# Optimization experiments

Measured on AMD Instinct MI355X. Metric: run time of the kernel, lower is better.

The kernel has to match this reference:

```python
import jax, jax.numpy as jnp
import numpy as np

EPS = 1e-5
NUM_GRAPHS = 32

def _bn(x, g, b):
    # BatchNorm1d, training mode: biased batch stats over the node axis
    mu = x.mean(0)
    var = ((x - mu) ** 2).mean(0)
    return g * (x - mu) * jax.lax.rsqrt(var + EPS) + b

def setup_inputs() -> dict:
    key = jax.random.key(0)
    ks = jax.random.split(key, 12)
    G, S, deg, D, L = 32, 1024, 32, 128, 4
    N, E = G * S, G * S * deg
    # within-graph random edges (proxy for radius_graph, no self-loops)
    rng = np.random.default_rng(0)
    col = np.repeat(np.arange(N), deg)                      # targets (x_i)
    src_local = (col % S + 1 + rng.integers(0, S - 1, size=E)) % S
    row = (col // S) * S + src_local                        # sources (x_j)
    edge_index = jnp.asarray(np.stack([row, col]).astype(np.int32))
    z = jax.random.randint(ks[0], (N,), 0, 100, dtype=jnp.int32)
    pos = jax.random.uniform(ks[1], (N, 3), dtype=jnp.float32) * 10.0
    batch = jnp.repeat(jnp.arange(G, dtype=jnp.int32), S)
    s_in = 1.0 / np.sqrt(2 * D + 1)
    s_d = 1.0 / np.sqrt(D)
    return {
        "z": z, "pos": pos, "batch": batch, "edge_index": edge_index,
        "emb": jax.random.normal(ks[2], (100, D), jnp.float32),
        "Wf": jax.random.normal(ks[3], (L, 2 * D + 1, D), jnp.float32) * s_in,
        "bf": jnp.zeros((L, D), jnp.float32),
        "Ws": jax.random.normal(ks[4], (L, 2 * D + 1, D), jnp.float32) * s_in,
        "bs": jnp.zeros((L, D), jnp.float32),
        "gc": jnp.ones((L, D), jnp.float32),
        "bc": jnp.zeros((L, D), jnp.float32),
        "gn": jnp.ones((L, D), jnp.float32),
        "bn_b": jnp.zeros((L, D), jnp.float32),
        "W1": jax.random.normal(ks[5], (D, D), jnp.float32) * s_d,
        "b1": jnp.zeros((D,), jnp.float32),
        "W2": jax.random.normal(ks[6], (D, 1), jnp.float32) * s_d,
        "b2": jnp.zeros((1,), jnp.float32),
    }

def reference(z, pos, batch, edge_index, emb, Wf, bf, Ws, bs, gc, bc, gn, bn_b, W1, b1, W2, b2):
    x = emb[z]                                              # [N, D]
    row, col = edge_index[0], edge_index[1]                 # j (src), i (tgt)
    dist = jnp.linalg.norm(pos[row] - pos[col], axis=-1, keepdims=True)  # [E,1]
    N = x.shape[0]
    for l in range(Wf.shape[0]):
        # CGConv message: cat([x_i, x_j, edge_attr]) -> gated softplus
        ze = jnp.concatenate([x[col], x[row], dist], axis=-1)  # [E, 2D+1]
        msg = jax.nn.sigmoid(ze @ Wf[l] + bf[l]) * jax.nn.softplus(ze @ Ws[l] + bs[l])
        agg = jax.ops.segment_sum(msg, col, num_segments=N)    # scatter-add to targets
        x = _bn(agg, gc[l], bc[l]) + x                         # CGConv internal BN + residual
        x = jax.nn.relu(_bn(x, gn[l], bn_b[l]))                # outer BN + ReLU (dropout=0)
    cnt = jax.ops.segment_sum(jnp.ones((N, 1), x.dtype), batch, num_segments=NUM_GRAPHS)
    g = jax.ops.segment_sum(x, batch, num_segments=NUM_GRAPHS) / cnt  # global_mean_pool
    h = jax.nn.relu(g @ W1 + b1)
    return (h @ W2 + b2).reshape(-1)
```

## Files before the change

kernel.cpp:

```cpp
#include <hip/hip_runtime.h>
#include <math.h>

#define D 128
#define LOG2E 1.44269504f

typedef short bf16x8 __attribute__((ext_vector_type(8)));
typedef float f32x4 __attribute__((ext_vector_type(4)));
typedef float f4 __attribute__((ext_vector_type(4)));
typedef unsigned short u16x4 __attribute__((ext_vector_type(4)));

__device__ __forceinline__ unsigned short f2bf(float f) {
    unsigned int u = __float_as_uint(f);
    u += 0x7fff + ((u >> 16) & 1);
    return (unsigned short)(u >> 16);
}
__device__ __forceinline__ float bf2f(unsigned short h) {
    return __uint_as_float(((unsigned int)h) << 16);
}
__device__ __forceinline__ bf16x8 load_bf8(const unsigned short* p) {
    return __builtin_bit_cast(bf16x8, *reinterpret_cast<const uint4*>(p));
}
__device__ __forceinline__ float exp2_hw(float x) {
    float r; asm("v_exp_f32 %0, %1" : "=v"(r) : "v"(x)); return r;
}
__device__ __forceinline__ float log2_hw(float x) {
    float r; asm("v_log_f32 %0, %1" : "=v"(r) : "v"(x)); return r;
}

__device__ __forceinline__ int swz_node0(int gi, int S, int G) {
    if ((G & 7) == 0 && (S & 7) == 0) {
        int xcd = gi & 7, i = gi >> 3;
        int bpg = S >> 3;
        int gr = i / bpg, li = i - gr * bpg;
        return (xcd + 8 * gr) * S + li * 8;
    }
    return gi * 8;
}

__global__ __launch_bounds__(256) void k_embed(const int* __restrict__ z,
        const float* __restrict__ emb, float* __restrict__ x,
        unsigned short* __restrict__ xh, unsigned short* __restrict__ xl, int N) {
    int idx = blockIdx.x * blockDim.x + threadIdx.x;
    if (idx >= N * 32) return;
    int n = idx >> 5;
    int d0 = (idx & 31) * 4;
    f4 v = *reinterpret_cast<const f4*>(emb + (size_t)z[n] * D + d0);
    *reinterpret_cast<f4*>(x + (size_t)n * D + d0) = v;
    u16x4 h, l;
    #pragma unroll
    for (int c = 0; c < 4; c++) {
        h[c] = f2bf(v[c]);
        l[c] = f2bf(v[c] - bf2f(h[c]));
    }
    *reinterpret_cast<u16x4*>(xh + (size_t)n * D + d0) = h;
    *reinterpret_cast<u16x4*>(xl + (size_t)n * D + d0) = l;
}

__global__ void k_dist(const int* __restrict__ row, const int* __restrict__ col,
                       const float* __restrict__ pos, int2* __restrict__ jd, int E) {
    int e = blockIdx.x * blockDim.x + threadIdx.x;
    if (e >= E) return;
    int r = row[e], c = col[e];
    float dx = pos[3 * r + 0] - pos[3 * c + 0];
    float dy = pos[3 * r + 1] - pos[3 * c + 1];
    float dz = pos[3 * r + 2] - pos[3 * c + 2];
    float dist = sqrtf(dx * dx + dy * dy + dz * dz);
    jd[e] = make_int2(r, __float_as_int(dist));
}

__global__ void k_cvtW(const float* __restrict__ Wf, const float* __restrict__ Ws,
                       unsigned short* __restrict__ Wth, unsigned short* __restrict__ Wtl,
                       int L) {
    int idx = blockIdx.x * blockDim.x + threadIdx.x;
    if (idx >= L * 4 * D * D) return;
    int k = idx & 127;
    int n = (idx >> 7) & 127;
    int mat = (idx >> 14) & 3;
    int l = idx >> 16;
    const float* src = (mat < 2) ? Wf : Ws;
    float scale = (mat < 2) ? -LOG2E : LOG2E;
    float v = scale * src[(size_t)l * 257 * D + (size_t)((mat & 1) * D + k) * D + n];
    unsigned short h = f2bf(v);
    Wth[idx] = h;
    Wtl[idx] = f2bf(v - bf2f(h));
}

__global__ __launch_bounds__(256) void k_gemm_mfma(
        const unsigned short* __restrict__ Xh, const unsigned short* __restrict__ Xl,
        const unsigned short* __restrict__ Wth, const unsigned short* __restrict__ Wtl,
        const float* __restrict__ bfl, const float* __restrict__ bsl,
        float* __restrict__ AfAs, float* __restrict__ BfBs, int S, int G) {
    int pair = blockIdx.y;
    float* O0 = AfAs + (pair ? 128 : 0);
    float* O1 = BfBs + (pair ? 128 : 0);
    const float* bias = pair ? bsl : bfl;
    float bsc = pair ? LOG2E : -LOG2E;
    const unsigned short* W0 = Wth + (size_t)(2 * pair) * D * D;
    const unsigned short* W1 = Wth + (size_t)(2 * pair + 1) * D * D;

    int wave = threadIdx.x >> 6;
    int lane = threadIdx.x & 63;
    int r16 = lane & 15;
    int kg = lane >> 4;

    int xb = blockIdx.x;
    int tile0;
    if ((G & 7) == 0 && (S & 127) == 0) {
        int xcd = xb & 7, i = xb >> 3;
        int tpg = S >> 7;
        int gi = i / tpg, t = i - gi * tpg;
        tile0 = (xcd + 8 * gi) * S + t * 128;
    } else tile0 = xb * 128;
    int row0 = tile0 + (wave >> 1) * 64;
    int wc = (wave & 1) * 64;

    f32x4 acc0[4][4], acc1[4][4];
    #pragma unroll
    for (int m = 0; m < 4; m++)
        #pragma unroll
        for (int n = 0; n < 4; n++) {
            acc0[m][n] = (f32x4){0.f, 0.f, 0.f, 0.f};
            acc1[m][n] = (f32x4){0.f, 0.f, 0.f, 0.f};
        }

    #pragma unroll
    for (int ks = 0; ks < 4; ++ks) {
        int k0 = ks * 32 + kg * 8;
        bf16x8 ah[4], al[4], b0[4], b1[4];
        #pragma unroll
        for (int m = 0; m < 4; m++) {
            size_t off = (size_t)(row0 + m * 16 + r16) * D + k0;
            ah[m] = load_bf8(Xh + off);
            al[m] = load_bf8(Xl + off);
        }
        #pragma unroll
        for (int n = 0; n < 4; n++) {
            size_t off = (size_t)(wc + n * 16 + r16) * D + k0;
            b0[n] = load_bf8(W0 + off);
            b1[n] = load_bf8(W1 + off);
        }
        #pragma unroll
        for (int m = 0; m < 4; m++)
            #pragma unroll
            for (int n = 0; n < 4; n++) {
                acc0[m][n] = __builtin_amdgcn_mfma_f32_16x16x32_bf16(ah[m], b0[n], acc0[m][n], 0, 0, 0);
                acc0[m][n] = __builtin_amdgcn_mfma_f32_16x16x32_bf16(al[m], b0[n], acc0[m][n], 0, 0, 0);
                acc1[m][n] = __builtin_amdgcn_mfma_f32_16x16x32_bf16(ah[m], b1[n], acc1[m][n], 0, 0, 0);
                acc1[m][n] = __builtin_amdgcn_mfma_f32_16x16x32_bf16(al[m], b1[n], acc1[m][n], 0, 0, 0);
            }
    }

    #pragma unroll
    for (int n = 0; n < 4; n++) {
        int col = wc + n * 16 + r16;
        float bv = bias[col] * bsc;
        #pragma unroll
        for (int m = 0; m < 4; m++) {
            int rbase = row0 + m * 16 + kg * 4;
            #pragma unroll
            for (int r = 0; r < 4; r++) {
                O0[(size_t)(rbase + r) * 256 + col] = acc0[m][n][r] + bv;
                O1[(size_t)(rbase + r) * 256 + col] = acc1[m][n][r];
            }
        }
    }
}

__global__ __launch_bounds__(256) void k_edges(
        const int2* __restrict__ jd,
        const float* __restrict__ AfAs, const float* __restrict__ BfBs,
        const float* __restrict__ wfd, const float* __restrict__ wsd,
        const float* __restrict__ x,
        float* __restrict__ agg, float* __restrict__ st, int N, int S, int G, int deg) {
    __shared__ int2 jds[512];
    __shared__ f4 sred[256];
    __shared__ f4 sredq[256];
    int b = blockIdx.x;
    int node0 = swz_node0(b, S, G);
    int tid = threadIdx.x;
    int grp = tid >> 5, lane = tid & 31;
    bool use_lds = (8 * deg) <= 512;
    if (use_lds) {
        int tot = 8 * deg;
        int lim = (node0 + 8 <= N) ? tot : (N > node0 ? (N - node0) * deg : 0);
        for (int t = tid; t < lim; t += 256) jds[t] = jd[(size_t)node0 * deg + t];
    }
    __syncthreads();
    int node = node0 + grp;
    bool active = node < N;
    int d0 = lane * 4;
    f4 acc = {0.f, 0.f, 0.f, 0.f};
    f4 xv = {0.f, 0.f, 0.f, 0.f};
    if (active) {
        const f4 af4 = *reinterpret_cast<const f4*>(AfAs + (size_t)node * 256 + d0);
        const f4 as4 = *reinterpret_cast<const f4*>(AfAs + (size_t)node * 256 + 128 + d0);
        const f4 wf4 = *reinterpret_cast<const f4*>(wfd + d0) * (-LOG2E);
        const f4 ws4 = *reinterpret_cast<const f4*>(wsd + d0) * (LOG2E);
        const int2* jrow = use_lds ? (jds + grp * deg) : (jd + (size_t)node * deg);
        #pragma unroll 8
        for (int e = 0; e < deg; e++) {
            int2 p = jrow[e];
            float dst = __int_as_float(p.y);
            int off = (p.x << 8) + d0;
            f4 bf4 = *reinterpret_cast<const f4*>(BfBs + off);
            f4 bs4 = *reinterpret_cast<const f4*>(BfBs + off + 128);
            #pragma unroll
            for (int c = 0; c < 4; c++) {
                float u2 = fmaf(dst, wf4[c], af4[c]) + bf4[c];
                float v2 = fmaf(dst, ws4[c], as4[c]) + bs4[c];
                float sE = exp2_hw(u2);
                float tE = exp2_hw(v2);
                float sg = __builtin_amdgcn_rcpf(1.0f + sE);
                float sp = log2_hw(1.0f + tE);
                acc[c] = fmaf(sg, sp, acc[c]);
            }
        }
        *reinterpret_cast<f4*>(agg + (size_t)node * D + d0) = acc;
        xv = *reinterpret_cast<const f4*>(x + (size_t)node * D + d0);
    }
    float* stb = st + (b & 7) * 640;
    sred[tid] = acc;
    sredq[tid] = acc * acc;
    __syncthreads();
    if (tid < 64) {
        int which = tid >> 5, l = tid & 31;
        f4 s = which ? sredq[l] : sred[l];
        #pragma unroll
        for (int g = 1; g < 8; g++) s += which ? sredq[g * 32 + l] : sred[g * 32 + l];
        float* dstp = stb + which * 128;
        #pragma unroll
        for (int c = 0; c < 4; c++) atomicAdd(dstp + l * 4 + c, s[c]);
    }
    __syncthreads();
    sred[tid] = xv;
    sredq[tid] = xv * xv;
    __syncthreads();
    if (tid < 64) {
        int which = tid >> 5, l = tid & 31;
        f4 s = which ? sredq[l] : sred[l];
        #pragma unroll
        for (int g = 1; g < 8; g++) s += which ? sredq[g * 32 + l] : sred[g * 32 + l];
        float* dstp = stb + 256 + which * 128;
        #pragma unroll
        for (int c = 0; c < 4; c++) atomicAdd(dstp + l * 4 + c, s[c]);
    }
    __syncthreads();
    sred[tid] = acc * xv;
    __syncthreads();
    if (tid < 32) {
        f4 s = sred[tid];
        #pragma unroll
        for (int g = 1; g < 8; g++) s += sred[g * 32 + tid];
        #pragma unroll
        for (int c = 0; c < 4; c++) atomicAdd(stb + 512 + tid * 4 + c, s[c]);
    }
}

__global__ __launch_bounds__(256) void k_bnfused(
        const float* __restrict__ st,
        const float* __restrict__ gc, const float* __restrict__ bc,
        const float* __restrict__ gn, const float* __restrict__ bnb,
        const float* __restrict__ agg, float* __restrict__ x,
        unsigned short* __restrict__ xh, unsigned short* __restrict__ xl,
        int N, int S, int G) {
    int tid = threadIdx.x;
    int lane = tid & 31, grp = tid >> 5;
    int d0 = lane * 4;
    int node = swz_node0(blockIdx.x, S, G) + grp;
    if (node >= N) return;
    float invN = 1.0f / (float)N;
    f4 Sa = {0.f, 0.f, 0.f, 0.f}, Sa2 = {0.f, 0.f, 0.f, 0.f};
    f4 Sx = {0.f, 0.f, 0.f, 0.f}, Sx2 = {0.f, 0.f, 0.f, 0.f}, Sax = {0.f, 0.f, 0.f, 0.f};
    #pragma unroll
    for (int r = 0; r < 8; r++) {
        const float* stb = st + r * 640;
        Sa  += *reinterpret_cast<const f4*>(stb + d0);
        Sa2 += *reinterpret_cast<const f4*>(stb + 128 + d0);
        Sx  += *reinterpret_cast<const f4*>(stb + 256 + d0);
        Sx2 += *reinterpret_cast<const f4*>(stb + 384 + d0);
        Sax += *reinterpret_cast<const f4*>(stb + 512 + d0);
    }
    f4 g1 = *reinterpret_cast<const f4*>(gc + d0);
    f4 b1v = *reinterpret_cast<const f4*>(bc + d0);
    f4 g2 = *reinterpret_cast<const f4*>(gn + d0);
    f4 b2v = *reinterpret_cast<const f4*>(bnb + d0);
    f4 A, C, mu2, inv2;
    #pragma unroll
    for (int c = 0; c < 4; c++) {
        float m1 = Sa[c] * invN;
        float var1 = Sa2[c] * invN - m1 * m1;
        float i1 = rsqrtf(var1 + 1e-5f);
        float a = g1[c] * i1;
        float cc = b1v[c] - a * m1;
        float mx = Sx[c] * invN;
        float m2 = b1v[c] + mx;
        float e2 = (a * a * Sa2[c] + 2.f * a * cc * Sa[c] + 2.f * a * Sax[c]
                    + 2.f * cc * Sx[c] + Sx2[c]) * invN + cc * cc;
        float var2 = e2 - m2 * m2;
        A[c] = a; C[c] = cc; mu2[c] = m2;
        inv2[c] = rsqrtf(var2 + 1e-5f);
    }
    size_t idx = (size_t)node * D + d0;
    f4 av = *reinterpret_cast<const f4*>(agg + idx);
    f4 xv = *reinterpret_cast<const f4*>(x + idx);
    f4 o;
    u16x4 h, l;
    #pragma unroll
    for (int c = 0; c < 4; c++) {
        float xn = fmaf(A[c], av[c], C[c]) + xv[c];
        float t = fmaf(g2[c] * (xn - mu2[c]), inv2[c], b2v[c]);
        t = fmaxf(t, 0.0f);
        o[c] = t;
        h[c] = f2bf(t);
        l[c] = f2bf(t - bf2f(h[c]));
    }
    *reinterpret_cast<f4*>(x + idx) = o;
    *reinterpret_cast<u16x4*>(xh + idx) = h;
    *reinterpret_cast<u16x4*>(xl + idx) = l;
}

__global__ __launch_bounds__(256) void k_pool(const float* __restrict__ x,
        float* __restrict__ gsum, int S, int G) {
    __shared__ f4 s[256];
    int b = blockIdx.x;
    int g, sub;
    if ((G & 31) == 0) { g = b & 31; sub = b >> 5; }
    else               { g = b >> 3; sub = b & 7; }
    int tid = threadIdx.x;
    int grp = tid >> 5, lane = tid & 31;
    int d0 = lane * 4;
    f4 a = {0.f, 0.f, 0.f, 0.f};
    for (int r = sub * 8 + grp; r < S; r += 64)
        a += *reinterpret_cast<const f4*>(x + ((size_t)g * S + r) * D + d0);
    s[tid] = a;
    __syncthreads();
    if (tid < 32) {
        f4 acc = s[tid];
        #pragma unroll
        for (int q = 1; q < 8; q++) acc += s[q * 32 + tid];
        #pragma unroll
        for (int c = 0; c < 4; c++) atomicAdd(&gsum[g * D + tid * 4 + c], acc[c]);
    }
}

__global__ __launch_bounds__(128) void k_mlp(const float* __restrict__ gsum,
        const float* __restrict__ W1, const float* __restrict__ b1,
        const float* __restrict__ W2, const float* __restrict__ b2,
        float* __restrict__ out, int S) {
    __shared__ float gm[D];
    __shared__ float red[128];
    int g = blockIdx.x, d = threadIdx.x;
    gm[d] = gsum[g * D + d] / (float)S;
    __syncthreads();
    float h = b1[d];
    #pragma unroll 8
    for (int k = 0; k < D; k++) h = fmaf(gm[k], W1[k * D + d], h);
    h = fmaxf(h, 0.0f);
    red[d] = h * W2[d];
    __syncthreads();
    for (int st = 64; st > 0; st >>= 1) {
        if (d < st) red[d] += red[d + st];
        __syncthreads();
    }
    if (d == 0) out[g] = red[0] + b2[0];
}

extern "C" void kernel_launch(void* const* d_in, const int* in_sizes, int n_in,
                              void* d_out, int out_size, void* d_ws, size_t ws_size,
                              hipStream_t stream) {
    const int*   z    = (const int*)d_in[0];
    const float* pos  = (const float*)d_in[1];
    const int*   eidx = (const int*)d_in[3];
    const float* emb  = (const float*)d_in[4];
    const float* Wf   = (const float*)d_in[5];
    const float* bf   = (const float*)d_in[6];
    const float* Ws   = (const float*)d_in[7];
    const float* bs   = (const float*)d_in[8];
    const float* gc   = (const float*)d_in[9];
    const float* bc   = (const float*)d_in[10];
    const float* gn   = (const float*)d_in[11];
    const float* bnb  = (const float*)d_in[12];
    const float* W1   = (const float*)d_in[13];
    const float* b1   = (const float*)d_in[14];
    const float* W2   = (const float*)d_in[15];
    const float* b2   = (const float*)d_in[16];

    int N = in_sizes[0];
    int E = in_sizes[3] / 2;
    int L = in_sizes[6] / D;
    int deg = E / N;
    int G = out_size;
    int S = N / G;

    const int* row = eidx;
    const int* col = eidx + E;

    float* ws = (float*)d_ws;
    size_t nd = (size_t)N * D;
    float* x    = ws;
    float* AfAs = x + nd;
    float* BfBs = AfAs + 2 * nd;
    float* agg  = BfBs + 2 * nd;
    int2*  jd   = (int2*)(agg + nd);
    unsigned short* xh  = (unsigned short*)(jd + E);
    unsigned short* xl  = xh + nd;
    unsigned short* Wth = xl + nd;
    unsigned short* Wtl = Wth + (size_t)L * 4 * D * D;
    float* stats = (float*)(Wtl + (size_t)L * 4 * D * D);
    float* gsum  = stats + (size_t)L * 5120;

    hipMemsetAsync(stats, 0, ((size_t)L * 5120 + (size_t)G * D) * sizeof(float), stream);

    k_cvtW<<<(L * 4 * D * D + 255) / 256, 256, 0, stream>>>(Wf, Ws, Wth, Wtl, L);
    k_embed<<<(N * 32 + 255) / 256, 256, 0, stream>>>(z, emb, x, xh, xl, N);
    k_dist<<<(E + 255) / 256, 256, 0, stream>>>(row, col, pos, jd, E);

    int NG = (N + 7) / 8;
    for (int l = 0; l < L; ++l) {
        const float* Wfl = Wf + (size_t)l * 257 * D;
        const float* Wsl = Ws + (size_t)l * 257 * D;
        float* stp = stats + (size_t)l * 5120;
        k_gemm_mfma<<<dim3(N / 128, 2), 256, 0, stream>>>(
            xh, xl, Wth + (size_t)l * 4 * D * D, Wtl + (size_t)l * 4 * D * D,
            bf + l * D, bs + l * D, AfAs, BfBs, S, G);
        k_edges<<<NG, 256, 0, stream>>>(jd, AfAs, BfBs, Wfl + 256 * D, Wsl + 256 * D,
                                        x, agg, stp, N, S, G, deg);
        k_bnfused<<<NG, 256, 0, stream>>>(stp, gc + l * D, bc + l * D,
                                          gn + l * D, bnb + l * D,
                                          agg, x, xh, xl, N, S, G);
    }
    k_pool<<<G * 8, 256, 0, stream>>>(x, gsum, S, G);
    k_mlp<<<G, 128, 0, stream>>>(gsum, W1, b1, W2, b2, (float*)d_out, S);
}
```

Measured before the change: 550.4 us.

## Merge setup kernels into one launch and pack edge math into float2 ops

Folds the embedding, edge-distance and weight-conversion kernels into a single k_setup launch that dispatches on block index, removing two kernel launches and their gaps. The edge index is stored pre-multiplied by 256, so the edge loop drops a shift. The per-edge pre-activation math is rewritten as two-wide float vectors so the compiler can emit packed FP32 FMA/add instructions. Any gain is limited to launch overhead and a few VALU ops inside an edge loop that is likely bound by the transcendental functions or memory.

Result: no change. 547.1 us (-0.6%).

```diff
diff --git a/kernel.cpp b/kernel.cpp
--- a/kernel.cpp
+++ b/kernel.cpp
@@ -7,6 +7,7 @@
 typedef short bf16x8 __attribute__((ext_vector_type(8)));
 typedef float f32x4 __attribute__((ext_vector_type(4)));
 typedef float f4 __attribute__((ext_vector_type(4)));
+typedef float f2v __attribute__((ext_vector_type(2)));
 typedef unsigned short u16x4 __attribute__((ext_vector_type(4)));
 
 __device__ __forceinline__ unsigned short f2bf(float f) {
@@ -37,52 +38,54 @@
     return gi * 8;
 }
 
-__global__ __launch_bounds__(256) void k_embed(const int* __restrict__ z,
-        const float* __restrict__ emb, float* __restrict__ x,
-        unsigned short* __restrict__ xh, unsigned short* __restrict__ xl, int N) {
-    int idx = blockIdx.x * blockDim.x + threadIdx.x;
-    if (idx >= N * 32) return;
-    int n = idx >> 5;
-    int d0 = (idx & 31) * 4;
-    f4 v = *reinterpret_cast<const f4*>(emb + (size_t)z[n] * D + d0);
-    *reinterpret_cast<f4*>(x + (size_t)n * D + d0) = v;
-    u16x4 h, l;
-    #pragma unroll
-    for (int c = 0; c < 4; c++) {
-        h[c] = f2bf(v[c]);
-        l[c] = f2bf(v[c] - bf2f(h[c]));
-    }
-    *reinterpret_cast<u16x4*>(xh + (size_t)n * D + d0) = h;
-    *reinterpret_cast<u16x4*>(xl + (size_t)n * D + d0) = l;
-}
-
-__global__ void k_dist(const int* __restrict__ row, const int* __restrict__ col,
-                       const float* __restrict__ pos, int2* __restrict__ jd, int E) {
-    int e = blockIdx.x * blockDim.x + threadIdx.x;
-    if (e >= E) return;
-    int r = row[e], c = col[e];
-    float dx = pos[3 * r + 0] - pos[3 * c + 0];
-    float dy = pos[3 * r + 1] - pos[3 * c + 1];
-    float dz = pos[3 * r + 2] - pos[3 * c + 2];
-    float dist = sqrtf(dx * dx + dy * dy + dz * dz);
-    jd[e] = make_int2(r, __float_as_int(dist));
-}
-
-__global__ void k_cvtW(const float* __restrict__ Wf, const float* __restrict__ Ws,
-                       unsigned short* __restrict__ Wth, unsigned short* __restrict__ Wtl,
-                       int L) {
-    int idx = blockIdx.x * blockDim.x + threadIdx.x;
-    if (idx >= L * 4 * D * D) return;
-    int k = idx & 127;
-    int n = (idx >> 7) & 127;
-    int mat = (idx >> 14) & 3;
-    int l = idx >> 16;
-    const float* src = (mat < 2) ? Wf : Ws;
-    float scale = (mat < 2) ? -LOG2E : LOG2E;
-    float v = scale * src[(size_t)l * 257 * D + (size_t)((mat & 1) * D + k) * D + n];
-    unsigned short h = f2bf(v);
-    Wth[idx] = h;
-    Wtl[idx] = f2bf(v - bf2f(h));
+__global__ __launch_bounds__(256) void k_setup(
+        const int* __restrict__ z, const float* __restrict__ emb,
+        float* __restrict__ x, unsigned short* __restrict__ xh,
+        unsigned short* __restrict__ xl,
+        const int* __restrict__ row, const int* __restrict__ col,
+        const float* __restrict__ pos, int2* __restrict__ jd,
+        const float* __restrict__ Wf, const float* __restrict__ Ws,
+        unsigned short* __restrict__ Wth, unsigned short* __restrict__ Wtl,
+        int N, int E, int L, int nb_embed, int nb_dist) {
+    int b = blockIdx.x;
+    if (b < nb_embed) {
+        int idx = b * 256 + threadIdx.x;
+        if (idx >= N * 32) return;
+        int n = idx >> 5;
+        int d0 = (idx & 31) * 4;
+        f4 v = *reinterpret_cast<const f4*>(emb + (size_t)z[n] * D + d0);
+        *reinterpret_cast<f4*>(x + (size_t)n * D + d0) = v;
+        u16x4 h, l;
+        #pragma unroll
+        for (int c = 0; c < 4; c++) {
+            h[c] = f2bf(v[c]);
+            l[c] = f2bf(v[c] - bf2f(h[c]));
+        }
+        *reinterpret_cast<u16x4*>(xh + (size_t)n * D + d0) = h;
+        *reinterpret_cast<u16x4*>(xl + (size_t)n * D + d0) = l;
+    } else if (b < nb_embed + nb_dist) {
+        int e = (b - nb_embed) * 256 + threadIdx.x;
+        if (e >= E) return;
+        int r = row[e], c = col[e];
+        float dx = pos[3 * r + 0] - pos[3 * c + 0];
+        float dy = pos[3 * r + 1] - pos[3 * c + 1];
+        float dz = pos[3 * r + 2] - pos[3 * c + 2];
+        float dist = sqrtf(dx * dx + dy * dy + dz * dz);
+        jd[e] = make_int2(r * 256, __float_as_int(dist));
+    } else {
+        int idx = (b - nb_embed - nb_dist) * 256 + threadIdx.x;
+        if (idx >= L * 4 * D * D) return;
+        int k = idx & 127;
+        int n = (idx >> 7) & 127;
+        int mat = (idx >> 14) & 3;
+        int l = idx >> 16;
+        const float* src = (mat < 2) ? Wf : Ws;
+        float scale = (mat < 2) ? -LOG2E : LOG2E;
+        float v = scale * src[(size_t)l * 257 * D + (size_t)((mat & 1) * D + k) * D + n];
+        unsigned short h = f2bf(v);
+        Wth[idx] = h;
+        Wtl[idx] = f2bf(v - bf2f(h));
+    }
 }
 
 __global__ __launch_bounds__(256) void k_gemm_mfma(
@@ -196,20 +199,33 @@
         const f4 as4 = *reinterpret_cast<const f4*>(AfAs + (size_t)node * 256 + 128 + d0);
         const f4 wf4 = *reinterpret_cast<const f4*>(wfd + d0) * (-LOG2E);
         const f4 ws4 = *reinterpret_cast<const f4*>(wsd + d0) * (LOG2E);
+        f2v af01 = __builtin_shufflevector(af4, af4, 0, 1);
+        f2v af23 = __builtin_shufflevector(af4, af4, 2, 3);
+        f2v as01 = __builtin_shufflevector(as4, as4, 0, 1);
+        f2v as23 = __builtin_shufflevector(as4, as4, 2, 3);
+        f2v wf01 = __builtin_shufflevector(wf4, wf4, 0, 1);
+        f2v wf23 = __builtin_shufflevector(wf4, wf4, 2, 3);
+        f2v ws01 = __builtin_shufflevector(ws4, ws4, 0, 1);
+        f2v ws23 = __builtin_shufflevector(ws4, ws4, 2, 3);
         const int2* jrow = use_lds ? (jds + grp * deg) : (jd + (size_t)node * deg);
         #pragma unroll 8
         for (int e = 0; e < deg; e++) {
             int2 p = jrow[e];
             float dst = __int_as_float(p.y);
-            int off = (p.x << 8) + d0;
+            int off = p.x + d0;
             f4 bf4 = *reinterpret_cast<const f4*>(BfBs + off);
             f4 bs4 = *reinterpret_cast<const f4*>(BfBs + off + 128);
+            f2v dst2 = {dst, dst};
+            f2v u01 = dst2 * wf01 + af01 + __builtin_shufflevector(bf4, bf4, 0, 1);
+            f2v u23 = dst2 * wf23 + af23 + __builtin_shufflevector(bf4, bf4, 2, 3);
+            f2v v01 = dst2 * ws01 + as01 + __builtin_shufflevector(bs4, bs4, 0, 1);
+            f2v v23 = dst2 * ws23 + as23 + __builtin_shufflevector(bs4, bs4, 2, 3);
+            float u[4] = {u01[0], u01[1], u23[0], u23[1]};
+            float v[4] = {v01[0], v01[1], v23[0], v23[1]};
             #pragma unroll
             for (int c = 0; c < 4; c++) {
-                float u2 = fmaf(dst, wf4[c], af4[c]) + bf4[c];
-                float v2 = fmaf(dst, ws4[c], as4[c]) + bs4[c];
-                float sE = exp2_hw(u2);
-                float tE = exp2_hw(v2);
+                float sE = exp2_hw(u[c]);
+                float tE = exp2_hw(v[c]);
                 float sg = __builtin_amdgcn_rcpf(1.0f + sE);
                 float sp = log2_hw(1.0f + tE);
                 acc[c] = fmaf(sg, sp, acc[c]);
@@ -411,9 +427,12 @@
 
     hipMemsetAsync(stats, 0, ((size_t)L * 5120 + (size_t)G * D) * sizeof(float), stream);
 
-    k_cvtW<<<(L * 4 * D * D + 255) / 256, 256, 0, stream>>>(Wf, Ws, Wth, Wtl, L);
-    k_embed<<<(N * 32 + 255) / 256, 256, 0, stream>>>(z, emb, x, xh, xl, N);
-    k_dist<<<(E + 255) / 256, 256, 0, stream>>>(row, col, pos, jd, E);
+    int nb_embed = (N * 32 + 255) / 256;
+    int nb_dist  = (E + 255) / 256;
+    int nb_cvtw  = (L * 4 * D * D + 255) / 256;
+    k_setup<<<nb_embed + nb_dist + nb_cvtw, 256, 0, stream>>>(
+        z, emb, x, xh, xl, row, col, pos, jd, Wf, Ws, Wth, Wtl,
+        N, E, L, nb_embed, nb_dist);
 
     int NG = (N + 7) / 8;
     for (int l = 0; l < L; ++l) {
```
